# Kernel tuning notes

Hardware: AMD Instinct MI355X
Metric: run time of the kernel (lower is better)

## Reference

```python
import jax, jax.numpy as jnp
import numpy as np

SIZE = 11
SIGMA = 1.5
PAD = 5

def _window2d():
    # cv2.getGaussianKernel(11, 1.5): normalized 1D Gaussian, outer product -> 2D window
    x = np.arange(SIZE) - (SIZE - 1) / 2.0
    g = np.exp(-(x * x) / (2.0 * SIGMA * SIGMA))
    g = g / g.sum()
    return jnp.asarray(np.outer(g, g), dtype=jnp.float32)

def _gconv(x, w):
    # x: [H, W]; replicate ('edge') pad by 5 then valid 11x11 correlation (matches torch
    # Conv2d with padding_mode='replicate'); output [H, W]
    xp = jnp.pad(x, PAD, mode='edge')[None, None]  # [1,1,H+10,W+10]
    y = jax.lax.conv_general_dilated(
        xp, w[None, None], window_strides=(1, 1), padding='VALID',
        dimension_numbers=('NCHW', 'OIHW', 'NCHW'))
    return y[0, 0]

def setup_inputs() -> dict:
    key = jax.random.key(0)
    k1, k2 = jax.random.split(key)
    H = W = 4096
    img1 = jax.random.uniform(k1, (H, W), dtype=jnp.float32) * 255.0
    img2 = jax.random.uniform(k2, (H, W), dtype=jnp.float32) * 255.0
    return {"img1": img1, "img2": img2}

def reference(img1, img2):
    w = _window2d()
    C1 = (0.01 * 255) ** 2
    C2 = (0.03 * 255) ** 2
    mu1 = _gconv(img1, w)
    mu2 = _gconv(img2, w)
    mu1_sq = mu1 * mu1
    mu2_sq = mu2 * mu2
    mu1_mu2 = mu1 * mu2
    sigma1_sq = _gconv(img1 * img1, w) - mu1_sq
    sigma2_sq = _gconv(img2 * img2, w) - mu2_sq
    sigma12 = _gconv(img1 * img2, w) - mu1_mu2
    ssim_map = (2 * mu1_mu2 + C1) * (2 * sigma12 + C2) / (
        (mu1_sq + mu2_sq + C1) * (sigma1_sq + sigma2_sq + C2))
    return jnp.mean(ssim_map)
```

## Files before the change

### kernel.cpp

```cpp
#include <hip/hip_runtime.h>
#include <cmath>

#define IMG_H 4096
#define IMG_W 4096
#define GX 8
#define GY 128
#define TCOLS 512
#define R 32
#define NITER (R + 10)
#define GOUT ((NITER + 10) / 11)
#define SWORDS 528
#define NF4 132
#define NSLOT (2*NF4)

struct GW { float w[11]; };

__device__ __forceinline__ int clampi(int v, int lo, int hi) {
  return v < lo ? lo : (v > hi ? hi : v);
}

__global__ __launch_bounds__(256, 2) void ssim_sweep_kernel(
    const float* __restrict__ img1, const float* __restrict__ img2,
    float* __restrict__ partial, GW gw) {
  __shared__ __align__(16) float sbuf[2][2][SWORDS];

  const int tid  = threadIdx.x;
  const int bx = blockIdx.x, by = blockIdx.y;
  const int c0   = bx * TCOLS;
  const int row0 = by * R;
  const bool edge = (bx == 0) || (bx == GX - 1);

  const int  j0   = tid;
  const bool has2 = (tid < NSLOT - 256);
  const int  j1   = tid + 256;

  auto load_slot = [&](int j, int gr) -> float4 {
    const float* img = (j < NF4) ? img1 : img2;
    int wo = ((j < NF4) ? j : j - NF4) * 4;
    long rowbase = (long)gr * IMG_W;
    int gc = c0 - 8 + wo;
    if (!edge) {
      return *reinterpret_cast<const float4*>(img + rowbase + gc);
    } else {
      float4 v;
      v.x = img[rowbase + clampi(gc + 0, 0, IMG_W - 1)];
      v.y = img[rowbase + clampi(gc + 1, 0, IMG_W - 1)];
      v.z = img[rowbase + clampi(gc + 2, 0, IMG_W - 1)];
      v.w = img[rowbase + clampi(gc + 3, 0, IMG_W - 1)];
      return v;
    }
  };
  auto store_slot = [&](int buf, int j, float4 v) {
    int im = (j < NF4) ? 0 : 1;
    int wo = ((j < NF4) ? j : j - NF4) * 4;
    *reinterpret_cast<float4*>(&sbuf[buf][im][wo]) = v;
  };

  {
    int gr = clampi(row0 - 5, 0, IMG_H - 1);
    float4 v0 = load_slot(j0, gr);
    store_slot(0, j0, v0);
    if (has2) { float4 v1 = load_slot(j1, gr); store_slot(0, j1, v1); }
  }

  float acc[4][11][2];
  float sum = 0.f;
  const float C1 = 6.5025f, C2 = 58.5225f;
  const int base = 2 * tid + 2;

  for (int g = 0; g < GOUT; ++g) {
    #pragma unroll
    for (int p = 0; p < 11; ++p) {
      const int i = g * 11 + p;
      if (i < NITER) {
        __syncthreads();

        float4 pre0, pre1;
        const bool pf = (i + 1 < NITER);
        if (pf) {
          int gr = clampi(row0 - 5 + i + 1, 0, IMG_H - 1);
          pre0 = load_slot(j0, gr);
          if (has2) pre1 = load_slot(j1, gr);
        }

        const int cur = i & 1;
        float wa[14], wb[14];
        #pragma unroll
        for (int m = 0; m < 7; ++m) {
          float2 fa = *reinterpret_cast<const float2*>(&sbuf[cur][0][base + 2 * m]);
          float2 fb = *reinterpret_cast<const float2*>(&sbuf[cur][1][base + 2 * m]);
          wa[2 * m] = fa.x; wa[2 * m + 1] = fa.y;
          wb[2 * m] = fb.x; wb[2 * m + 1] = fb.y;
        }

        float h[4][2];
        #pragma unroll
        for (int ch = 0; ch < 4; ++ch) { h[ch][0] = 0.f; h[ch][1] = 0.f; }
        #pragma unroll
        for (int e = 1; e <= 12; ++e) {
          const float a = wa[e], b = wb[e];
          const float sq = fmaf(b, b, a * a);
          const float ab = a * b;
          if (e <= 11) {
            const float w0 = gw.w[e - 1];
            h[0][0] = fmaf(w0, a,  h[0][0]);
            h[1][0] = fmaf(w0, b,  h[1][0]);
            h[2][0] = fmaf(w0, sq, h[2][0]);
            h[3][0] = fmaf(w0, ab, h[3][0]);
          }
          if (e >= 2) {
            const float w1 = gw.w[e - 2];
            h[0][1] = fmaf(w1, a,  h[0][1]);
            h[1][1] = fmaf(w1, b,  h[1][1]);
            h[2][1] = fmaf(w1, sq, h[2][1]);
            h[3][1] = fmaf(w1, ab, h[3][1]);
          }
        }

        #pragma unroll
        for (int m = 0; m <= 10; ++m) {
          const int s = (p + 1 + m) % 11;
          const float wd = gw.w[10 - m];
          if (m == 10) {
            #pragma unroll
            for (int ch = 0; ch < 4; ++ch) {
              acc[ch][s][0] = wd * h[ch][0];
              acc[ch][s][1] = wd * h[ch][1];
            }
          } else {
            #pragma unroll
            for (int ch = 0; ch < 4; ++ch) {
              acc[ch][s][0] = fmaf(wd, h[ch][0], acc[ch][s][0]);
              acc[ch][s][1] = fmaf(wd, h[ch][1], acc[ch][s][1]);
            }
          }
        }

        if (i >= 10) {
          const int cs = (p + 1) % 11;
          #pragma unroll
          for (int x = 0; x < 2; ++x) {
            float mu1 = acc[0][cs][x], mu2 = acc[1][cs][x];
            float s3  = acc[2][cs][x], s4  = acc[3][cs][x];
            float mu1s = mu1 * mu1, mu2s = mu2 * mu2, m12 = mu1 * mu2;
            float num = (2.f * m12 + C1) * (2.f * (s4 - m12) + C2);
            float den = (mu1s + mu2s + C1) * ((s3 - mu1s - mu2s) + C2);
            sum += num * __builtin_amdgcn_rcpf(den);
          }
        }

        if (pf) {
          store_slot((i + 1) & 1, j0, pre0);
          if (has2) store_slot((i + 1) & 1, j1, pre1);
        }
      }
    }
  }

  #pragma unroll
  for (int off = 32; off > 0; off >>= 1) sum += __shfl_down(sum, off);
  __shared__ float wsum[4];
  if ((tid & 63) == 0) wsum[tid >> 6] = sum;
  __syncthreads();
  if (tid == 0)
    partial[by * GX + bx] = wsum[0] + wsum[1] + wsum[2] + wsum[3];
}

__global__ __launch_bounds__(256) void ssim_reduce_kernel(
    const float* __restrict__ partial, float* __restrict__ out) {
  int tid = threadIdx.x;
  double s = (double)partial[tid] + (double)partial[tid + 256] +
             (double)partial[tid + 512] + (double)partial[tid + 768];
  #pragma unroll
  for (int off = 32; off > 0; off >>= 1) s += __shfl_down(s, off);
  __shared__ double ws[4];
  if ((tid & 63) == 0) ws[tid >> 6] = s;
  __syncthreads();
  if (tid == 0)
    out[0] = (float)((ws[0] + ws[1] + ws[2] + ws[3]) /
                     ((double)IMG_H * (double)IMG_W));
}

extern "C" void kernel_launch(void* const* d_in, const int* in_sizes, int n_in,
                              void* d_out, int out_size, void* d_ws, size_t ws_size,
                              hipStream_t stream) {
  const float* img1 = (const float*)d_in[0];
  const float* img2 = (const float*)d_in[1];
  float* partial = (float*)d_ws;
  float* out = (float*)d_out;

  GW gw;
  double g[11], s = 0.0;
  for (int i = 0; i < 11; ++i) {
    double x = i - 5.0;
    g[i] = exp(-(x * x) / (2.0 * 1.5 * 1.5));
    s += g[i];
  }
  for (int i = 0; i < 11; ++i) gw.w[i] = (float)(g[i] / s);

  dim3 grid(GX, GY);
  ssim_sweep_kernel<<<grid, 256, 0, stream>>>(img1, img2, partial, gw);
  ssim_reduce_kernel<<<1, 256, 0, stream>>>(partial, out);
}
```

Measured before the change: 208.0 us.

## Give each wavefront a private column strip and LDS buffer, drop block barriers

Splits each block's 512-column tile into four 128-column strips, one per wavefront. Each wavefront loads its own halo into a private double-buffered LDS region, which lets the kernel drop the per-row __syncthreads and rely on intra-wave ordering. This removes block-wide synchronisation stalls between the four waves. In exchange, each wavefront redundantly loads its own 16-column halo, and correctness now depends on LDS store/load ordering within a wave without an explicit barrier.

After: 200.8 us. 3.5% less time.

```diff
diff --git a/kernel.cpp b/kernel.cpp
--- a/kernel.cpp
+++ b/kernel.cpp
@@ -6,12 +6,13 @@
 #define GX 8
 #define GY 128
 #define TCOLS 512
+#define WCOLS 128
 #define R 32
 #define NITER (R + 10)
 #define GOUT ((NITER + 10) / 11)
-#define SWORDS 528
-#define NF4 132
-#define NSLOT (2*NF4)
+#define SWORDS_W 144
+#define NF4W 36
+#define NSLOTW (2*NF4W)
 
 struct GW { float w[11]; };
 
@@ -22,23 +23,25 @@
 __global__ __launch_bounds__(256, 2) void ssim_sweep_kernel(
     const float* __restrict__ img1, const float* __restrict__ img2,
     float* __restrict__ partial, GW gw) {
-  __shared__ __align__(16) float sbuf[2][2][SWORDS];
+  __shared__ __align__(16) float sbuf[4][2][2][SWORDS_W];
 
   const int tid  = threadIdx.x;
+  const int wv   = tid >> 6;
+  const int lane = tid & 63;
   const int bx = blockIdx.x, by = blockIdx.y;
-  const int c0   = bx * TCOLS;
+  const int cw   = bx * TCOLS + wv * WCOLS;
   const int row0 = by * R;
-  const bool edge = (bx == 0) || (bx == GX - 1);
-
-  const int  j0   = tid;
-  const bool has2 = (tid < NSLOT - 256);
-  const int  j1   = tid + 256;
+  const bool edge = (cw == 0) || (cw + WCOLS == IMG_W);
+
+  const int  j0   = lane;
+  const bool has2 = (lane < NSLOTW - 64);
+  const int  j1   = lane + 64;
 
   auto load_slot = [&](int j, int gr) -> float4 {
-    const float* img = (j < NF4) ? img1 : img2;
-    int wo = ((j < NF4) ? j : j - NF4) * 4;
+    const float* img = (j < NF4W) ? img1 : img2;
+    int wo = ((j < NF4W) ? j : j - NF4W) * 4;
     long rowbase = (long)gr * IMG_W;
-    int gc = c0 - 8 + wo;
+    int gc = cw - 8 + wo;
     if (!edge) {
       return *reinterpret_cast<const float4*>(img + rowbase + gc);
     } else {
@@ -51,9 +54,9 @@
     }
   };
   auto store_slot = [&](int buf, int j, float4 v) {
-    int im = (j < NF4) ? 0 : 1;
-    int wo = ((j < NF4) ? j : j - NF4) * 4;
-    *reinterpret_cast<float4*>(&sbuf[buf][im][wo]) = v;
+    int im = (j < NF4W) ? 0 : 1;
+    int wo = ((j < NF4W) ? j : j - NF4W) * 4;
+    *reinterpret_cast<float4*>(&sbuf[wv][buf][im][wo]) = v;
   };
 
   {
@@ -66,15 +69,13 @@
   float acc[4][11][2];
   float sum = 0.f;
   const float C1 = 6.5025f, C2 = 58.5225f;
-  const int base = 2 * tid + 2;
+  const int base = 2 * lane + 2;
 
   for (int g = 0; g < GOUT; ++g) {
     #pragma unroll
     for (int p = 0; p < 11; ++p) {
       const int i = g * 11 + p;
       if (i < NITER) {
-        __syncthreads();
-
         float4 pre0, pre1;
         const bool pf = (i + 1 < NITER);
         if (pf) {
@@ -87,8 +88,8 @@
         float wa[14], wb[14];
         #pragma unroll
         for (int m = 0; m < 7; ++m) {
-          float2 fa = *reinterpret_cast<const float2*>(&sbuf[cur][0][base + 2 * m]);
-          float2 fb = *reinterpret_cast<const float2*>(&sbuf[cur][1][base + 2 * m]);
+          float2 fa = *reinterpret_cast<const float2*>(&sbuf[wv][cur][0][base + 2 * m]);
+          float2 fb = *reinterpret_cast<const float2*>(&sbuf[wv][cur][1][base + 2 * m]);
           wa[2 * m] = fa.x; wa[2 * m + 1] = fa.y;
           wb[2 * m] = fb.x; wb[2 * m + 1] = fb.y;
         }
@@ -160,7 +161,7 @@
   #pragma unroll
   for (int off = 32; off > 0; off >>= 1) sum += __shfl_down(sum, off);
   __shared__ float wsum[4];
-  if ((tid & 63) == 0) wsum[tid >> 6] = sum;
+  if (lane == 0) wsum[wv] = sum;
   __syncthreads();
   if (tid == 0)
     partial[by * GX + bx] = wsum[0] + wsum[1] + wsum[2] + wsum[3];
```
